# Kernel optimization log

Hardware: AMD Instinct MI355X
Metric: run time of the kernel (lower is better)

## Reference

```python
import jax, jax.numpy as jnp
import numpy as np

N_NODES = 10000
N_EDGES = 160000
MUL = 128            # channel multiplicity
N_SPECIES = 4        # node_attrs scalars
N_RADIAL = 8         # edge_feats scalars
AVG_NEIGH = 16.0
SQRT3 = 1.7320508075688772


def setup_inputs() -> dict:
    key = jax.random.key(0)
    ks = jax.random.split(key, 16)
    inp = {}
    inp['node_attrs'] = jax.random.uniform(ks[0], (N_NODES, N_SPECIES), dtype=jnp.float32)
    inp['node_feats'] = jax.random.normal(ks[1], (N_NODES, MUL * 4), dtype=jnp.float32)  # 128x0e + 128x1o
    inp['edge_attrs'] = jax.random.normal(ks[2], (N_EDGES, 4), dtype=jnp.float32)        # 1x0e + 1x1o (SH lmax=1)
    inp['edge_feats'] = jax.random.normal(ks[3], (N_EDGES, N_RADIAL), dtype=jnp.float32)
    inp['edge_index'] = jax.random.randint(ks[4], (2, N_EDGES), 0, N_NODES, dtype=jnp.int32)
    # linear_up: per-l mixing (o3.Linear on 128x0e+128x1o)
    inp['W_up0'] = jax.random.normal(ks[5], (MUL, MUL), dtype=jnp.float32)
    inp['W_up1'] = jax.random.normal(ks[6], (MUL, MUL), dtype=jnp.float32)
    # radial MLP [8, 64, 64, 512] (conv_tp.weight_numel = 4 instructions * 128)
    inp['W_mlp1'] = jax.random.normal(ks[7], (N_RADIAL, 64), dtype=jnp.float32)
    inp['W_mlp2'] = jax.random.normal(ks[8], (64, 64), dtype=jnp.float32)
    inp['W_mlp3'] = jax.random.normal(ks[9], (64, 4 * MUL), dtype=jnp.float32)
    # linear: irreps_mid.simplify() = 256x0e + 256x1o -> 128x0e + 128x1o
    inp['W_lin0'] = jax.random.normal(ks[10], (2 * MUL, MUL), dtype=jnp.float32)
    inp['W_lin1'] = jax.random.normal(ks[11], (2 * MUL, MUL), dtype=jnp.float32)
    # skip_tp: FullyConnectedTensorProduct(target, 4x0e -> target), uvw weights per l
    inp['W_skip0'] = jax.random.normal(ks[12], (MUL, N_SPECIES, MUL), dtype=jnp.float32)
    inp['W_skip1'] = jax.random.normal(ks[13], (MUL, N_SPECIES, MUL), dtype=jnp.float32)
    inp['update_coeff_param'] = jnp.zeros((1,), dtype=jnp.float32)
    return inp


def reference(node_attrs, node_feats, edge_attrs, edge_feats, edge_index,
              W_up0, W_up1, W_mlp1, W_mlp2, W_mlp3, W_lin0, W_lin1,
              W_skip0, W_skip1, update_coeff_param):
    N = node_feats.shape[0]
    # split node feats into irrep blocks: scalars [N,128], vectors [N,128,3]
    s = node_feats[:, :MUL]
    v = node_feats[:, MUL:].reshape(N, MUL, 3)
    # linear_up (o3.Linear, fan-in normalized)
    inv_up = 1.0 / jnp.sqrt(jnp.float32(MUL))
    s = (s @ W_up0) * inv_up
    v = jnp.einsum('nui,uw->nwi', v, W_up1) * inv_up
    # radial MLP -> per-edge TP weights (e3nn FullyConnectedNet style, fan-in normalized, silu)
    h = jax.nn.silu((edge_feats @ W_mlp1) / jnp.sqrt(jnp.float32(N_RADIAL)))
    h = jax.nn.silu((h @ W_mlp2) / jnp.sqrt(jnp.float32(64)))
    tpw = (h @ W_mlp3) / jnp.sqrt(jnp.float32(64))  # [E, 512]
    # instruction order (sorted by output irrep): 0e*0e->0e, 1o*1o->0e, 0e*1o->1o, 1o*0e->1o
    w_a, w_b, w_c, w_d = tpw[:, :MUL], tpw[:, MUL:2*MUL], tpw[:, 2*MUL:3*MUL], tpw[:, 3*MUL:]
    sender, receiver = edge_index[0], edge_index[1]
    xs = s[sender]          # [E,128] gather
    xv = v[sender]          # [E,128,3]
    ea_s = edge_attrs[:, :1]    # [E,1]
    ea_v = edge_attrs[:, 1:4]   # [E,3]
    # CG tensor-product messages ('uvu', component norm)
    m0 = w_a * xs * ea_s                                        # 0e x 0e -> 0e
    m1 = w_b * (jnp.einsum('eui,ei->eu', xv, ea_v) / SQRT3)      # 1o x 1o -> 0e
    m2 = (w_c * xs)[:, :, None] * ea_v[:, None, :]               # 0e x 1o -> 1o
    m3 = w_d[:, :, None] * xv * ea_s[:, :, None]                 # 1o x 0e -> 1o
    ms = jnp.concatenate([m0, m1], axis=1)                       # [E,256]
    mv = jnp.concatenate([m2, m3], axis=1)                       # [E,256,3]
    # scatter-sum to receiver nodes
    Ms = jax.ops.segment_sum(ms, receiver, num_segments=N)       # [N,256]
    Mv = jax.ops.segment_sum(mv, receiver, num_segments=N)       # [N,256,3]
    # linear (256x0e+256x1o -> 128x0e+128x1o), divided by avg_num_neighbors
    inv_lin = 1.0 / (jnp.sqrt(jnp.float32(2 * MUL)) * AVG_NEIGH)
    S = (Ms @ W_lin0) * inv_lin                                  # [N,128]
    V = jnp.einsum('nui,uw->nwi', Mv, W_lin1) * inv_lin          # [N,128,3]
    # skip_tp: FullyConnectedTensorProduct(message, node_attrs) with uvw weights
    inv_sk = 1.0 / jnp.sqrt(jnp.float32(MUL * N_SPECIES))
    sc_s = jnp.einsum('nu,nv,uvw->nw', S, node_attrs, W_skip0) * inv_sk
    sc_v = jnp.einsum('nui,nv,uvw->nwi', V, node_attrs, W_skip1) * inv_sk
    # residual stream mixing (sc=False branch)
    c = jax.nn.sigmoid(update_coeff_param)                       # [1]
    c_old = jax.lax.rsqrt(c * c + 1.0)
    c_new = c * c_old
    S = c_old * S + c_new * sc_s
    V = c_old * V + c_new * sc_v
    # reshape_irreps: [N, mul, 1 + 3]
    out = jnp.concatenate([S[:, :, None], V], axis=-1)           # [N,128,4]
    return out
```

## Files before the change

### kernel.cpp

```cpp
#include <hip/hip_runtime.h>

#define MUL 128

typedef __attribute__((ext_vector_type(8))) short bf16x8;
typedef __attribute__((ext_vector_type(4))) short bf16x4;
typedef __attribute__((ext_vector_type(4))) float f32x4;

__device__ __constant__ float kINV_UP   = 0.08838834764831845f;
__device__ __constant__ float kINV_L1   = 0.35355339059327373f;
__device__ __constant__ float kINV_L2   = 0.125f;
__device__ __constant__ float kINV_L3   = 0.125f;
__device__ __constant__ float kINV_LIN  = 0.00390625f;
__device__ __constant__ float kINV_SK   = 0.044194173824159216f;
__device__ __constant__ float kINV_SQ3  = 0.5773502691896258f;

#define WAVE_LDS_SYNC() asm volatile("s_waitcnt lgkmcnt(0)" ::: "memory")

static __device__ __forceinline__ short f2bf(float f) {
  unsigned u = __float_as_uint(f);
  unsigned r = (u + 0x7FFFu + ((u >> 16) & 1u)) >> 16;
  return (short)r;
}

__global__ __launch_bounds__(256) void k_cvtcnt(
    const float* __restrict__ W_up0, const float* __restrict__ W_up1,
    const float* __restrict__ W_lin0, const float* __restrict__ W_lin1,
    const float* __restrict__ W_sk0, const float* __restrict__ W_sk1,
    const float* __restrict__ W_mlp2, const float* __restrict__ W_mlp3,
    short* __restrict__ W0T, short* __restrict__ W1T,
    short* __restrict__ Wl0T, short* __restrict__ Wl1T,
    short* __restrict__ Wsk0T, short* __restrict__ Wsk1T,
    short* __restrict__ W2T, short* __restrict__ W3T,
    const int* __restrict__ eidx, int* __restrict__ cnt, int E, int CVT_B) {
  int blk = blockIdx.x;
  if (blk >= CVT_B) {
    int e = (blk - CVT_B) * 256 + threadIdx.x;
    if (e < E) atomicAdd(&cnt[eidx[E + e]], 1);
    return;
  }
  int id = blk * 256 + threadIdx.x;
  if (id < 16384) {
    int w = id >> 7, u = id & 127;
    W0T[id] = f2bf(W_up0[u * 128 + w]);
    return;
  }
  id -= 16384;
  if (id < 16384) {
    int w = id >> 7, u = id & 127;
    W1T[id] = f2bf(W_up1[u * 128 + w]);
    return;
  }
  id -= 16384;
  if (id < 32768) {
    int w = id >> 8, u = id & 255;
    Wl0T[id] = f2bf(W_lin0[u * 128 + w]);
    return;
  }
  id -= 32768;
  if (id < 32768) {
    int w = id >> 8, u = id & 255;
    Wl1T[id] = f2bf(W_lin1[u * 128 + w]);
    return;
  }
  id -= 32768;
  if (id < 65536) {
    int w = id >> 9, k = id & 511;
    int v = k >> 7, u = k & 127;
    Wsk0T[id] = f2bf(W_sk0[(u * 4 + v) * 128 + w]);
    return;
  }
  id -= 65536;
  if (id < 65536) {
    int w = id >> 9, k = id & 511;
    int v = k >> 7, u = k & 127;
    Wsk1T[id] = f2bf(W_sk1[(u * 4 + v) * 128 + w]);
    return;
  }
  id -= 65536;
  if (id < 4096) {
    int c = id >> 6, k = id & 63;
    W2T[id] = f2bf(W_mlp2[k * 64 + c]);
    return;
  }
  id -= 4096;
  if (id < 32768) {
    int c = id >> 6, k = id & 63;
    W3T[id] = f2bf(W_mlp3[k * 512 + c]);
  }
}

__global__ __launch_bounds__(1024) void k_scan(const int* __restrict__ cnt,
                                               int* __restrict__ offs,
                                               int* __restrict__ cursor, int N) {
  __shared__ int part[1024];
  const int t = threadIdx.x;
  int CH = (N + 1023) >> 10;
  if (CH > 16) CH = 16;
  const int base = t * CH;
  int loc[16];
  int s = 0;
  for (int i = 0; i < CH; ++i) {
    int idx = base + i;
    loc[i] = (idx < N) ? cnt[idx] : 0;
    s += loc[i];
  }
  part[t] = s;
  __syncthreads();
  for (int off = 1; off < 1024; off <<= 1) {
    int v = part[t];
    int add = (t >= off) ? part[t - off] : 0;
    __syncthreads();
    part[t] = v + add;
    __syncthreads();
  }
  int excl = part[t] - s;
  for (int i = 0; i < CH; ++i) {
    int idx = base + i;
    if (idx < N) { offs[idx] = excl; cursor[idx] = excl; }
    excl += loc[i];
  }
  if (t == 1023) offs[N] = part[1023];
}

__global__ __launch_bounds__(256) void k_fused3(
    const int* __restrict__ eidx, int* __restrict__ cursor, int* __restrict__ sorted,
    const float* __restrict__ nf, const short* __restrict__ W0T,
    const short* __restrict__ W1T, float* __restrict__ s_up, float* __restrict__ v_up,
    const float* __restrict__ ef, const float* __restrict__ W1f,
    const short* __restrict__ W2T, const short* __restrict__ W3T,
    unsigned* __restrict__ tpw2, int N, int E, int MLP_B, int UP_B) {
  __shared__ __align__(16) char smem[48128];
  const int t = threadIdx.x;
  int blk = blockIdx.x;

  if (blk < MLP_B) {
    float* sW1  = (float*)smem;
    short* sW2T = (short*)(smem + 2048);
    short* sh1  = (short*)(smem + 11264);
    short* sh2  = (short*)(smem + 29696);

    for (int i = t * 4; i < 512; i += 1024)
      *reinterpret_cast<float4*>(&sW1[i]) = *reinterpret_cast<const float4*>(W1f + i);
    for (int i = t * 8; i < 4096; i += 2048) {
      int r = i >> 6, c = i & 63;
      *reinterpret_cast<bf16x8*>(&sW2T[r * 72 + c]) =
          *reinterpret_cast<const bf16x8*>(&W2T[r * 64 + c]);
    }
    __syncthreads();

    const int w = t >> 6, l = t & 63, li = l & 15, g = l >> 4;
    const int eb = blk * 128 + w * 32;
    const int es0 = eb + li, es1 = eb + 16 + li;
    short* h1r0 = sh1 + (w * 32 + li) * 72;
    short* h1r1 = sh1 + (w * 32 + 16 + li) * 72;
    short* h2r0 = sh2 + (w * 32 + li) * 72;
    short* h2r1 = sh2 + (w * 32 + 16 + li) * 72;

    {
#pragma unroll
      for (int s = 0; s < 2; ++s) {
        const int e = s ? es1 : es0;
        short* h1row = s ? h1r1 : h1r0;
        float4 qa = {0.f, 0.f, 0.f, 0.f}, qb = {0.f, 0.f, 0.f, 0.f};
        if (e < E) {
          qa = *reinterpret_cast<const float4*>(ef + (size_t)e * 8);
          qb = *reinterpret_cast<const float4*>(ef + (size_t)e * 8 + 4);
        }
        const float x[8] = {qa.x, qa.y, qa.z, qa.w, qb.x, qb.y, qb.z, qb.w};
        bf16x8 p0, p1;
#pragma unroll
        for (int j = 0; j < 16; ++j) {
          int col = g * 16 + j;
          float a = 0.f;
#pragma unroll
          for (int k = 0; k < 8; ++k) a += x[k] * sW1[k * 64 + col];
          a *= kINV_L1;
          short hv = f2bf(a / (1.f + __expf(-a)));
          if (j < 8) p0[j] = hv; else p1[j - 8] = hv;
        }
        *reinterpret_cast<bf16x8*>(&h1row[g * 16])     = p0;
        *reinterpret_cast<bf16x8*>(&h1row[g * 16 + 8]) = p1;
      }
    }
    WAVE_LDS_SYNC();

    {
      bf16x8 hb0[2], hb1[2];
      hb0[0] = *reinterpret_cast<const bf16x8*>(&h1r0[g * 8]);
      hb1[0] = *reinterpret_cast<const bf16x8*>(&h1r0[32 + g * 8]);
      hb0[1] = *reinterpret_cast<const bf16x8*>(&h1r1[g * 8]);
      hb1[1] = *reinterpret_cast<const bf16x8*>(&h1r1[32 + g * 8]);
#pragma unroll
      for (int ct = 0; ct < 4; ++ct) {
        const short* wrow = &sW2T[(ct * 16 + li) * 72];
        bf16x8 a0 = *reinterpret_cast<const bf16x8*>(&wrow[g * 8]);
        bf16x8 a1 = *reinterpret_cast<const bf16x8*>(&wrow[32 + g * 8]);
#pragma unroll
        for (int s = 0; s < 2; ++s) {
          f32x4 acc = {0.f, 0.f, 0.f, 0.f};
          acc = __builtin_amdgcn_mfma_f32_16x16x32_bf16(a0, hb0[s], acc, 0, 0, 0);
          acc = __builtin_amdgcn_mfma_f32_16x16x32_bf16(a1, hb1[s], acc, 0, 0, 0);
          bf16x4 hq;
#pragma unroll
          for (int r = 0; r < 4; ++r) {
            float a = acc[r] * kINV_L2;
            hq[r] = f2bf(a / (1.f + __expf(-a)));
          }
          *reinterpret_cast<bf16x4*>(&((s ? h2r1 : h2r0)[ct * 16 + g * 4])) = hq;
        }
      }
    }
    WAVE_LDS_SYNC();

    {
      bf16x8 b0[2], b1[2];
      b0[0] = *reinterpret_cast<const bf16x8*>(&h2r0[g * 8]);
      b1[0] = *reinterpret_cast<const bf16x8*>(&h2r0[32 + g * 8]);
      b0[1] = *reinterpret_cast<const bf16x8*>(&h2r1[g * 8]);
      b1[1] = *reinterpret_cast<const bf16x8*>(&h2r1[32 + g * 8]);
      const bool ok0 = es0 < E, ok1 = es1 < E;

      bf16x8 c0, c1, c2, c3;
      {
        const int rowA = li;
        c0 = *reinterpret_cast<const bf16x8*>(&W3T[(size_t)rowA * 64 + g * 8]);
        c1 = *reinterpret_cast<const bf16x8*>(&W3T[(size_t)rowA * 64 + 32 + g * 8]);
        c2 = *reinterpret_cast<const bf16x8*>(&W3T[(size_t)(rowA + 256) * 64 + g * 8]);
        c3 = *reinterpret_cast<const bf16x8*>(&W3T[(size_t)(rowA + 256) * 64 + 32 + g * 8]);
      }
#pragma unroll
      for (int rt = 0; rt < 16; ++rt) {
        bf16x8 n0, n1, n2, n3;
        const bool pf = (rt < 15);
        if (pf) {
          const int rowA = (rt + 1) * 16 + li;
          n0 = *reinterpret_cast<const bf16x8*>(&W3T[(size_t)rowA * 64 + g * 8]);
          n1 = *reinterpret_cast<const bf16x8*>(&W3T[(size_t)rowA * 64 + 32 + g * 8]);
          n2 = *reinterpret_cast<const bf16x8*>(&W3T[(size_t)(rowA + 256) * 64 + g * 8]);
          n3 = *reinterpret_cast<const bf16x8*>(&W3T[(size_t)(rowA + 256) * 64 + 32 + g * 8]);
        }
#pragma unroll
        for (int s = 0; s < 2; ++s) {
          f32x4 accA = {0.f, 0.f, 0.f, 0.f};
          f32x4 accB = {0.f, 0.f, 0.f, 0.f};
          accA = __builtin_amdgcn_mfma_f32_16x16x32_bf16(c0, b0[s], accA, 0, 0, 0);
          accA = __builtin_amdgcn_mfma_f32_16x16x32_bf16(c1, b1[s], accA, 0, 0, 0);
          accB = __builtin_amdgcn_mfma_f32_16x16x32_bf16(c2, b0[s], accB, 0, 0, 0);
          accB = __builtin_amdgcn_mfma_f32_16x16x32_bf16(c3, b1[s], accB, 0, 0, 0);
          if (s ? ok1 : ok0) {
            uint4 d;
            unsigned* dp = &d.x;
#pragma unroll
            for (int r = 0; r < 4; ++r) {
              unsigned lo = (unsigned)(unsigned short)f2bf(accA[r] * kINV_L3);
              unsigned hi = (unsigned)(unsigned short)f2bf(accB[r] * kINV_L3);
              dp[r] = lo | (hi << 16);
            }
            *reinterpret_cast<uint4*>(
                &tpw2[(size_t)(s ? es1 : es0) * 256 + rt * 16 + g * 4]) = d;
          }
        }
        if (pf) { c0 = n0; c1 = n1; c2 = n2; c3 = n3; }
      }
    }
    return;
  }
  blk -= MLP_B;

  if (blk < UP_B) {
    short* lsA = (short*)smem;
    const int nb = blk * 16;

    for (int base = t * 8; base < 16 * 512; base += 256 * 8) {
      int n = base >> 9, j0 = base & 511;
      float vals[8];
      if (nb + n < N) {
        float4 q0 = *reinterpret_cast<const float4*>(nf + (size_t)(nb + n) * 512 + j0);
        float4 q1 = *reinterpret_cast<const float4*>(nf + (size_t)(nb + n) * 512 + j0 + 4);
        vals[0] = q0.x; vals[1] = q0.y; vals[2] = q0.z; vals[3] = q0.w;
        vals[4] = q1.x; vals[5] = q1.y; vals[6] = q1.z; vals[7] = q1.w;
      } else {
#pragma unroll
        for (int e = 0; e < 8; ++e) vals[e] = 0.f;
      }
#pragma unroll
      for (int e = 0; e < 8; ++e) {
        int idx = j0 + e;
        if (idx < 128) {
          lsA[(0 * 16 + n) * 136 + idx] = f2bf(vals[e]);
        } else {
          unsigned q = idx - 128;
          unsigned u = q / 3u;
          unsigned i = q - u * 3u;
          lsA[((1 + i) * 16 + n) * 136 + u] = f2bf(vals[e]);
        }
      }
    }
    __syncthreads();

    const int c = t >> 6;
    const int lane = t & 63;
    const int col = lane & 15;
    const int g = lane >> 4;

    const short* WT = c ? W1T : W0T;

    bf16x8 af[4];
#pragma unroll
    for (int kk = 0; kk < 4; ++kk)
      af[kk] = *reinterpret_cast<const bf16x8*>(&lsA[(c * 16 + col) * 136 + kk * 32 + g * 8]);

#pragma unroll
    for (int nt = 0; nt < 8; ++nt) {
      f32x4 acc = {0.f, 0.f, 0.f, 0.f};
#pragma unroll
      for (int kk = 0; kk < 4; ++kk) {
        bf16x8 bf = *reinterpret_cast<const bf16x8*>(&WT[(size_t)(nt * 16 + col) * 128 + kk * 32 + g * 8]);
        acc = __builtin_amdgcn_mfma_f32_16x16x32_bf16(af[kk], bf, acc, 0, 0, 0);
      }
#pragma unroll
      for (int r = 0; r < 4; ++r) {
        int nd = nb + g * 4 + r;
        if (nd < N) {
          float val = acc[r] * kINV_UP;
          if (c == 0) s_up[(size_t)nd * 128 + nt * 16 + col] = val;
          else        v_up[(size_t)nd * 384 + (c - 1) * 128 + nt * 16 + col] = val;
        }
      }
    }
    return;
  }
  blk -= UP_B;

  int e = blk * 256 + t;
  if (e < E) {
    int r = eidx[E + e];
    int p = atomicAdd(&cursor[r], 1);
    sorted[p] = e;
  }
}

__global__ __launch_bounds__(256) void k_gather(
    const int* __restrict__ sorted, const int* __restrict__ offs,
    const unsigned* __restrict__ tpw2, const float* __restrict__ eattr,
    const int* __restrict__ eidx,
    const float* __restrict__ s_up, const float* __restrict__ v_up,
    float* __restrict__ Ms, float* __restrict__ Mv, int N, int SB) {
  const int t = threadIdx.x;
  const int vside = blockIdx.x >= SB;
  const int nb = (vside ? blockIdx.x - SB : blockIdx.x) * 4;
  const int n = nb + (t >> 6);
  if (n >= N) return;
  const int l = t & 63;
  const int u0 = l * 2;

  float aMs0 = 0.f, aMs1 = 0.f;
  float aV[3][2] = {};

  const int e0 = offs[n], e1 = offs[n + 1];

  if (!vside) {
    for (int p = e0; p < e1; ++p) {
      int eid = sorted[p];
      int snd = eidx[eid];
      float4 ea = *reinterpret_cast<const float4*>(eattr + (size_t)eid * 4);
      uint2 q = *reinterpret_cast<const uint2*>(tpw2 + (size_t)eid * 256 + u0);
      float2 xs = *reinterpret_cast<const float2*>(s_up + (size_t)snd * 128 + u0);
      float tA0 = __uint_as_float(q.x << 16);
      float tB0 = __uint_as_float(q.x & 0xFFFF0000u);
      float tA1 = __uint_as_float(q.y << 16);
      float tB1 = __uint_as_float(q.y & 0xFFFF0000u);
      float xe0 = xs.x * ea.x, xe1 = xs.y * ea.x;
      aMs0 += tA0 * xe0;
      aMs1 += tA1 * xe1;
      float wc0 = tB0 * xs.x, wc1 = tB1 * xs.y;
      aV[0][0] += wc0 * ea.y; aV[0][1] += wc1 * ea.y;
      aV[1][0] += wc0 * ea.z; aV[1][1] += wc1 * ea.z;
      aV[2][0] += wc0 * ea.w; aV[2][1] += wc1 * ea.w;
    }
    *reinterpret_cast<float2*>(Ms + (size_t)n * 256 + u0) = make_float2(aMs0, aMs1);
#pragma unroll
    for (int i = 0; i < 3; ++i)
      *reinterpret_cast<float2*>(Mv + (size_t)n * 768 + i * 256 + u0) =
          make_float2(aV[i][0], aV[i][1]);
  } else {
    for (int p = e0; p < e1; ++p) {
      int eid = sorted[p];
      int snd = eidx[eid];
      float4 ea = *reinterpret_cast<const float4*>(eattr + (size_t)eid * 4);
      uint2 q = *reinterpret_cast<const uint2*>(tpw2 + (size_t)eid * 256 + 128 + u0);
      const float* xv = v_up + (size_t)snd * 384 + u0;
      float2 x0 = *reinterpret_cast<const float2*>(xv);
      float2 x1 = *reinterpret_cast<const float2*>(xv + 128);
      float2 x2 = *reinterpret_cast<const float2*>(xv + 256);
      float tA0 = __uint_as_float(q.x << 16);
      float tB0 = __uint_as_float(q.x & 0xFFFF0000u);
      float tA1 = __uint_as_float(q.y << 16);
      float tB1 = __uint_as_float(q.y & 0xFFFF0000u);
      float dot0 = x0.x * ea.y + x1.x * ea.z + x2.x * ea.w;
      float dot1 = x0.y * ea.y + x1.y * ea.z + x2.y * ea.w;
      aMs0 += tA0 * dot0 * kINV_SQ3;
      aMs1 += tA1 * dot1 * kINV_SQ3;
      float wd0 = tB0 * ea.x, wd1 = tB1 * ea.x;
      aV[0][0] += wd0 * x0.x; aV[0][1] += wd1 * x0.y;
      aV[1][0] += wd0 * x1.x; aV[1][1] += wd1 * x1.y;
      aV[2][0] += wd0 * x2.x; aV[2][1] += wd1 * x2.y;
    }
    *reinterpret_cast<float2*>(Ms + (size_t)n * 256 + 128 + u0) = make_float2(aMs0, aMs1);
#pragma unroll
    for (int i = 0; i < 3; ++i)
      *reinterpret_cast<float2*>(Mv + (size_t)n * 768 + i * 256 + 128 + u0) =
          make_float2(aV[i][0], aV[i][1]);
  }
}

__global__ __launch_bounds__(256) void k_linskip(
    const float* __restrict__ Ms, const float* __restrict__ Mv,
    const short* __restrict__ Wl0T, const short* __restrict__ Wl1T,
    const short* __restrict__ Wsk0T, const short* __restrict__ Wsk1T,
    const float* __restrict__ attrs, const float* __restrict__ upd,
    float* __restrict__ out, int N) {
  __shared__ __align__(16) short lsA[4][16][264];
  __shared__ __align__(16) short lsS[4][16][136];
  __shared__ float sat[16][4];
  const int nb = blockIdx.x * 16;
  const int t = threadIdx.x;

  for (int base = t * 4; base < 16 * 1024; base += 1024) {
    int n = base >> 10, j = base & 1023;
    int comp = j >> 8, u = j & 255;
    float4 q = {0.f, 0.f, 0.f, 0.f};
    if (nb + n < N) {
      const float* src = (comp == 0) ? (Ms + (size_t)(nb + n) * 256 + u)
                                     : (Mv + (size_t)(nb + n) * 768 + (size_t)(comp - 1) * 256 + u);
      q = *reinterpret_cast<const float4*>(src);
    }
    lsA[comp][n][u + 0] = f2bf(q.x);
    lsA[comp][n][u + 1] = f2bf(q.y);
    lsA[comp][n][u + 2] = f2bf(q.z);
    lsA[comp][n][u + 3] = f2bf(q.w);
  }
  if (t < 64) {
    int n = t >> 2, v = t & 3;
    sat[n][v] = (nb + n < N) ? attrs[(size_t)(nb + n) * 4 + v] : 0.f;
  }
  __syncthreads();

  const int c = t >> 6;
  const int lane = t & 63;
  const int col = lane & 15;
  const int g = lane >> 4;

  const short* WLT = c ? Wl1T : Wl0T;
  const short* WST = c ? Wsk1T : Wsk0T;

  bf16x8 af1[8];
#pragma unroll
  for (int kk = 0; kk < 8; ++kk)
    af1[kk] = *reinterpret_cast<const bf16x8*>(&lsA[c][col][kk * 32 + g * 8]);

  f32x4 Sreg[8];
#pragma unroll
  for (int nt = 0; nt < 8; ++nt) {
    f32x4 acc = {0.f, 0.f, 0.f, 0.f};
#pragma unroll
    for (int kk = 0; kk < 8; ++kk) {
      bf16x8 bf = *reinterpret_cast<const bf16x8*>(&WLT[(size_t)(nt * 16 + col) * 256 + kk * 32 + g * 8]);
      acc = __builtin_amdgcn_mfma_f32_16x16x32_bf16(af1[kk], bf, acc, 0, 0, 0);
    }
#pragma unroll
    for (int r = 0; r < 4; ++r) acc[r] *= kINV_LIN;
    Sreg[nt] = acc;
#pragma unroll
    for (int r = 0; r < 4; ++r)
      lsS[c][g * 4 + r][nt * 16 + col] = f2bf(acc[r]);
  }

  float satr[4][4];
#pragma unroll
  for (int r = 0; r < 4; ++r)
#pragma unroll
    for (int v = 0; v < 4; ++v) satr[r][v] = sat[g * 4 + r][v];

  __syncthreads();

  bf16x8 af2[4];
#pragma unroll
  for (int kk = 0; kk < 4; ++kk)
    af2[kk] = *reinterpret_cast<const bf16x8*>(&lsS[c][col][kk * 32 + g * 8]);

  const float p = upd[0];
  const float cc = 1.f / (1.f + __expf(-p));
  const float c_old = rsqrtf(cc * cc + 1.f);
  const float c_new = cc * c_old;

#pragma unroll
  for (int nt = 0; nt < 8; ++nt) {
    float fin[4] = {0.f, 0.f, 0.f, 0.f};
#pragma unroll
    for (int v = 0; v < 4; ++v) {
      f32x4 tmp = {0.f, 0.f, 0.f, 0.f};
#pragma unroll
      for (int kk = 0; kk < 4; ++kk) {
        bf16x8 bf = *reinterpret_cast<const bf16x8*>(&WST[(size_t)(nt * 16 + col) * 512 + v * 128 + kk * 32 + g * 8]);
        tmp = __builtin_amdgcn_mfma_f32_16x16x32_bf16(af2[kk], bf, tmp, 0, 0, 0);
      }
#pragma unroll
      for (int r = 0; r < 4; ++r) fin[r] += satr[r][v] * tmp[r];
    }
#pragma unroll
    for (int r = 0; r < 4; ++r) {
      int nd = nb + g * 4 + r;
      if (nd < N) {
        float val = c_old * Sreg[nt][r] + c_new * fin[r] * kINV_SK;
        out[((size_t)nd * 128 + nt * 16 + col) * 4 + c] = val;
      }
    }
  }
}

extern "C" void kernel_launch(void* const* d_in, const int* in_sizes, int n_in,
                              void* d_out, int out_size, void* d_ws, size_t ws_size,
                              hipStream_t stream) {
  const float* node_attrs = (const float*)d_in[0];
  const float* node_feats = (const float*)d_in[1];
  const float* edge_attrs = (const float*)d_in[2];
  const float* edge_feats = (const float*)d_in[3];
  const int*   edge_index = (const int*)d_in[4];
  const float* W_up0  = (const float*)d_in[5];
  const float* W_up1  = (const float*)d_in[6];
  const float* W_mlp1 = (const float*)d_in[7];
  const float* W_mlp2 = (const float*)d_in[8];
  const float* W_mlp3 = (const float*)d_in[9];
  const float* W_lin0 = (const float*)d_in[10];
  const float* W_lin1 = (const float*)d_in[11];
  const float* W_skip0 = (const float*)d_in[12];
  const float* W_skip1 = (const float*)d_in[13];
  const float* upd = (const float*)d_in[14];
  float* out = (float*)d_out;

  const int N = in_sizes[0] / 4;
  const int E = in_sizes[4] / 2;

  float* ws = (float*)d_ws;
  float* s_up = ws;
  float* v_up = s_up + (size_t)N * 128;
  float* Ms   = v_up + (size_t)N * 384;
  float* Mv   = Ms + (size_t)N * 256;
  int* cnt    = (int*)(Mv + (size_t)N * 768);
  int* offs   = cnt + N;
  int* cursor = offs + N + 1;
  int* sorted = cursor + N;

  short* wbase = (short*)((((uintptr_t)(sorted + E)) + 15) & ~(uintptr_t)15);
  short* W0T   = wbase;
  short* W1T   = W0T + 16384;
  short* Wl0T  = W1T + 16384;
  short* Wl1T  = Wl0T + 32768;
  short* Wsk0T = Wl1T + 32768;
  short* Wsk1T = Wsk0T + 65536;
  short* W2T   = Wsk1T + 65536;
  short* W3T   = W2T + 4096;
  unsigned* tpw2 = (unsigned*)(W3T + 32768);

  const int CVT_B = (266240 + 255) / 256;
  const int CNT_B = (E + 255) / 256;
  const int MLP_B = (E + 127) / 128;
  const int UP_B  = (N + 15) / 16;
  const int SC_B  = (E + 255) / 256;
  const int SB    = (N + 3) / 4;

  hipMemsetAsync(cnt, 0, (size_t)N * sizeof(int), stream);

  k_cvtcnt<<<CVT_B + CNT_B, 256, 0, stream>>>(
      W_up0, W_up1, W_lin0, W_lin1, W_skip0, W_skip1, W_mlp2, W_mlp3,
      W0T, W1T, Wl0T, Wl1T, Wsk0T, Wsk1T, W2T, W3T,
      edge_index, cnt, E, CVT_B);
  k_scan<<<1, 1024, 0, stream>>>(cnt, offs, cursor, N);
  k_fused3<<<MLP_B + UP_B + SC_B, 256, 0, stream>>>(
      edge_index, cursor, sorted,
      node_feats, W0T, W1T, s_up, v_up,
      edge_feats, W_mlp1, W2T, W3T, tpw2, N, E, MLP_B, UP_B);
  k_gather<<<2 * SB, 256, 0, stream>>>(sorted, offs, tpw2, edge_attrs, edge_index,
                                       s_up, v_up, Ms, Mv, N, SB);
  k_linskip<<<(N + 15) / 16, 256, 0, stream>>>(Ms, Mv, Wl0T, Wl1T, Wsk0T, Wsk1T,
                                               node_attrs, upd, out, N);
}
```

Before: 282.2 us.

## Merge scalar/vector gather passes, store sender in sorted records, prefetch next edge

The counting-sort step now stores (edge id, sender) pairs, so the gather no longer does a dependent lookup into edge_index. The separate scalar and vector gather blocks are merged into one block per node group, so each edge's record, attrs and tpw2 row are read once. Loads for the next edge are software-prefetched while the current one is being accumulated. The cost is more registers per thread and half as many blocks, which may lower occupancy and latency hiding.

```diff
diff --git a/kernel.cpp b/kernel.cpp
--- a/kernel.cpp
+++ b/kernel.cpp
@@ -123,7 +123,7 @@
 }
 
 __global__ __launch_bounds__(256) void k_fused3(
-    const int* __restrict__ eidx, int* __restrict__ cursor, int* __restrict__ sorted,
+    const int* __restrict__ eidx, int* __restrict__ cursor, uint2* __restrict__ recs,
     const float* __restrict__ nf, const short* __restrict__ W0T,
     const short* __restrict__ W1T, float* __restrict__ s_up, float* __restrict__ v_up,
     const float* __restrict__ ef, const float* __restrict__ W1f,
@@ -335,82 +335,95 @@
   int e = blk * 256 + t;
   if (e < E) {
     int r = eidx[E + e];
+    int snd = eidx[e];
     int p = atomicAdd(&cursor[r], 1);
-    sorted[p] = e;
+    recs[p] = make_uint2((unsigned)e, (unsigned)snd);
   }
 }
 
 __global__ __launch_bounds__(256) void k_gather(
-    const int* __restrict__ sorted, const int* __restrict__ offs,
+    const uint2* __restrict__ recs, const int* __restrict__ offs,
     const unsigned* __restrict__ tpw2, const float* __restrict__ eattr,
-    const int* __restrict__ eidx,
     const float* __restrict__ s_up, const float* __restrict__ v_up,
-    float* __restrict__ Ms, float* __restrict__ Mv, int N, int SB) {
+    float* __restrict__ Ms, float* __restrict__ Mv, int N) {
   const int t = threadIdx.x;
-  const int vside = blockIdx.x >= SB;
-  const int nb = (vside ? blockIdx.x - SB : blockIdx.x) * 4;
-  const int n = nb + (t >> 6);
+  const int n = blockIdx.x * 4 + (t >> 6);
   if (n >= N) return;
   const int l = t & 63;
   const int u0 = l * 2;
 
-  float aMs0 = 0.f, aMs1 = 0.f;
-  float aV[3][2] = {};
+  float aMsS0 = 0.f, aMsS1 = 0.f;
+  float aMsV0 = 0.f, aMsV1 = 0.f;
+  float aVs[3][2] = {};
+  float aVv[3][2] = {};
 
   const int e0 = offs[n], e1 = offs[n + 1];
 
-  if (!vside) {
+  if (e0 < e1) {
+    const int last = e1 - 1;
+    uint2 rec_c = recs[e0];
+    uint2 rec_n = recs[min(e0 + 1, last)];
+    float4 ea_c = *reinterpret_cast<const float4*>(eattr + (size_t)rec_c.x * 4);
+    uint2 qs_c = *reinterpret_cast<const uint2*>(tpw2 + (size_t)rec_c.x * 256 + u0);
+    uint2 qv_c = *reinterpret_cast<const uint2*>(tpw2 + (size_t)rec_c.x * 256 + 128 + u0);
+    float2 xs_c = *reinterpret_cast<const float2*>(s_up + (size_t)rec_c.y * 128 + u0);
+    const float* xvp = v_up + (size_t)rec_c.y * 384 + u0;
+    float2 x0_c = *reinterpret_cast<const float2*>(xvp);
+    float2 x1_c = *reinterpret_cast<const float2*>(xvp + 128);
+    float2 x2_c = *reinterpret_cast<const float2*>(xvp + 256);
+
     for (int p = e0; p < e1; ++p) {
-      int eid = sorted[p];
-      int snd = eidx[eid];
-      float4 ea = *reinterpret_cast<const float4*>(eattr + (size_t)eid * 4);
-      uint2 q = *reinterpret_cast<const uint2*>(tpw2 + (size_t)eid * 256 + u0);
-      float2 xs = *reinterpret_cast<const float2*>(s_up + (size_t)snd * 128 + u0);
-      float tA0 = __uint_as_float(q.x << 16);
-      float tB0 = __uint_as_float(q.x & 0xFFFF0000u);
-      float tA1 = __uint_as_float(q.y << 16);
-      float tB1 = __uint_as_float(q.y & 0xFFFF0000u);
-      float xe0 = xs.x * ea.x, xe1 = xs.y * ea.x;
-      aMs0 += tA0 * xe0;
-      aMs1 += tA1 * xe1;
-      float wc0 = tB0 * xs.x, wc1 = tB1 * xs.y;
-      aV[0][0] += wc0 * ea.y; aV[0][1] += wc1 * ea.y;
-      aV[1][0] += wc0 * ea.z; aV[1][1] += wc1 * ea.z;
-      aV[2][0] += wc0 * ea.w; aV[2][1] += wc1 * ea.w;
-    }
-    *reinterpret_cast<float2*>(Ms + (size_t)n * 256 + u0) = make_float2(aMs0, aMs1);
-#pragma unroll
-    for (int i = 0; i < 3; ++i)
-      *reinterpret_cast<float2*>(Mv + (size_t)n * 768 + i * 256 + u0) =
-          make_float2(aV[i][0], aV[i][1]);
-  } else {
-    for (int p = e0; p < e1; ++p) {
-      int eid = sorted[p];
-      int snd = eidx[eid];
-      float4 ea = *reinterpret_cast<const float4*>(eattr + (size_t)eid * 4);
-      uint2 q = *reinterpret_cast<const uint2*>(tpw2 + (size_t)eid * 256 + 128 + u0);
-      const float* xv = v_up + (size_t)snd * 384 + u0;
-      float2 x0 = *reinterpret_cast<const float2*>(xv);
-      float2 x1 = *reinterpret_cast<const float2*>(xv + 128);
-      float2 x2 = *reinterpret_cast<const float2*>(xv + 256);
-      float tA0 = __uint_as_float(q.x << 16);
-      float tB0 = __uint_as_float(q.x & 0xFFFF0000u);
-      float tA1 = __uint_as_float(q.y << 16);
-      float tB1 = __uint_as_float(q.y & 0xFFFF0000u);
-      float dot0 = x0.x * ea.y + x1.x * ea.z + x2.x * ea.w;
-      float dot1 = x0.y * ea.y + x1.y * ea.z + x2.y * ea.w;
-      aMs0 += tA0 * dot0 * kINV_SQ3;
-      aMs1 += tA1 * dot1 * kINV_SQ3;
-      float wd0 = tB0 * ea.x, wd1 = tB1 * ea.x;
-      aV[0][0] += wd0 * x0.x; aV[0][1] += wd1 * x0.y;
-      aV[1][0] += wd0 * x1.x; aV[1][1] += wd1 * x1.y;
-      aV[2][0] += wd0 * x2.x; aV[2][1] += wd1 * x2.y;
-    }
-    *reinterpret_cast<float2*>(Ms + (size_t)n * 256 + 128 + u0) = make_float2(aMs0, aMs1);
-#pragma unroll
-    for (int i = 0; i < 3; ++i)
-      *reinterpret_cast<float2*>(Mv + (size_t)n * 768 + i * 256 + 128 + u0) =
-          make_float2(aV[i][0], aV[i][1]);
+      float4 ea_n = *reinterpret_cast<const float4*>(eattr + (size_t)rec_n.x * 4);
+      uint2 qs_n = *reinterpret_cast<const uint2*>(tpw2 + (size_t)rec_n.x * 256 + u0);
+      uint2 qv_n = *reinterpret_cast<const uint2*>(tpw2 + (size_t)rec_n.x * 256 + 128 + u0);
+      float2 xs_n = *reinterpret_cast<const float2*>(s_up + (size_t)rec_n.y * 128 + u0);
+      const float* xvn = v_up + (size_t)rec_n.y * 384 + u0;
+      float2 x0_n = *reinterpret_cast<const float2*>(xvn);
+      float2 x1_n = *reinterpret_cast<const float2*>(xvn + 128);
+      float2 x2_n = *reinterpret_cast<const float2*>(xvn + 256);
+      uint2 rec_n2 = recs[min(p + 2, last)];
+
+      {
+        float tA0 = __uint_as_float(qs_c.x << 16);
+        float tB0 = __uint_as_float(qs_c.x & 0xFFFF0000u);
+        float tA1 = __uint_as_float(qs_c.y << 16);
+        float tB1 = __uint_as_float(qs_c.y & 0xFFFF0000u);
+        aMsS0 += tA0 * xs_c.x * ea_c.x;
+        aMsS1 += tA1 * xs_c.y * ea_c.x;
+        float wc0 = tB0 * xs_c.x, wc1 = tB1 * xs_c.y;
+        aVs[0][0] += wc0 * ea_c.y; aVs[0][1] += wc1 * ea_c.y;
+        aVs[1][0] += wc0 * ea_c.z; aVs[1][1] += wc1 * ea_c.z;
+        aVs[2][0] += wc0 * ea_c.w; aVs[2][1] += wc1 * ea_c.w;
+      }
+      {
+        float tA0 = __uint_as_float(qv_c.x << 16);
+        float tB0 = __uint_as_float(qv_c.x & 0xFFFF0000u);
+        float tA1 = __uint_as_float(qv_c.y << 16);
+        float tB1 = __uint_as_float(qv_c.y & 0xFFFF0000u);
+        float dot0 = x0_c.x * ea_c.y + x1_c.x * ea_c.z + x2_c.x * ea_c.w;
+        float dot1 = x0_c.y * ea_c.y + x1_c.y * ea_c.z + x2_c.y * ea_c.w;
+        aMsV0 += tA0 * dot0 * kINV_SQ3;
+        aMsV1 += tA1 * dot1 * kINV_SQ3;
+        float wd0 = tB0 * ea_c.x, wd1 = tB1 * ea_c.x;
+        aVv[0][0] += wd0 * x0_c.x; aVv[0][1] += wd1 * x0_c.y;
+        aVv[1][0] += wd0 * x1_c.x; aVv[1][1] += wd1 * x1_c.y;
+        aVv[2][0] += wd0 * x2_c.x; aVv[2][1] += wd1 * x2_c.y;
+      }
+
+      ea_c = ea_n; qs_c = qs_n; qv_c = qv_n; xs_c = xs_n;
+      x0_c = x0_n; x1_c = x1_n; x2_c = x2_n;
+      rec_n = rec_n2;
+    }
+  }
+
+  *reinterpret_cast<float2*>(Ms + (size_t)n * 256 + u0)       = make_float2(aMsS0, aMsS1);
+  *reinterpret_cast<float2*>(Ms + (size_t)n * 256 + 128 + u0) = make_float2(aMsV0, aMsV1);
+#pragma unroll
+  for (int i = 0; i < 3; ++i) {
+    *reinterpret_cast<float2*>(Mv + (size_t)n * 768 + i * 256 + u0) =
+        make_float2(aVs[i][0], aVs[i][1]);
+    *reinterpret_cast<float2*>(Mv + (size_t)n * 768 + i * 256 + 128 + u0) =
+        make_float2(aVv[i][0], aVv[i][1]);
   }
 }
 
@@ -550,9 +563,9 @@
   int* cnt    = (int*)(Mv + (size_t)N * 768);
   int* offs   = cnt + N;
   int* cursor = offs + N + 1;
-  int* sorted = cursor + N;
-
-  short* wbase = (short*)((((uintptr_t)(sorted + E)) + 15) & ~(uintptr_t)15);
+  uint2* recs = (uint2*)((((uintptr_t)(cursor + N)) + 7) & ~(uintptr_t)7);
+
+  short* wbase = (short*)((((uintptr_t)(recs + E)) + 15) & ~(uintptr_t)15);
   short* W0T   = wbase;
   short* W1T   = W0T + 16384;
   short* Wl0T  = W1T + 16384;
@@ -568,7 +581,6 @@
   const int MLP_B = (E + 127) / 128;
   const int UP_B  = (N + 15) / 16;
   const int SC_B  = (E + 255) / 256;
-  const int SB    = (N + 3) / 4;
 
   hipMemsetAsync(cnt, 0, (size_t)N * sizeof(int), stream);
 
@@ -578,11 +590,11 @@
       edge_index, cnt, E, CVT_B);
   k_scan<<<1, 1024, 0, stream>>>(cnt, offs, cursor, N);
   k_fused3<<<MLP_B + UP_B + SC_B, 256, 0, stream>>>(
-      edge_index, cursor, sorted,
+      edge_index, cursor, recs,
       node_feats, W0T, W1T, s_up, v_up,
       edge_feats, W_mlp1, W2T, W3T, tpw2, N, E, MLP_B, UP_B);
-  k_gather<<<2 * SB, 256, 0, stream>>>(sorted, offs, tpw2, edge_attrs, edge_index,
-                                       s_up, v_up, Ms, Mv, N, SB);
+  k_gather<<<(N + 3) / 4, 256, 0, stream>>>(recs, offs, tpw2, edge_attrs,
+                                            s_up, v_up, Ms, Mv, N);
   k_linskip<<<(N + 15) / 16, 256, 0, stream>>>(Ms, Mv, Wl0T, Wl1T, Wsk0T, Wsk1T,
                                                node_attrs, upd, out, N);
 }
```

Measured after the change: 277.4 us. Within noise of the previous version (-1.7%).
